# Kernel tuning notes

Measured on AMD Instinct MI355X. Metric: run time of the kernel, lower is better.

Reference implementation:

```python
import jax, jax.numpy as jnp
import numpy as np

B, T_ENC, T_DEC = 64, 256, 200
MEL, R = 80, 2
ENC_DIM = 256   # must equal attention_context_dim (context = weighted sum of encoder outputs)
ATT = 256       # attention_rnn_units == attention_context_dim
DEC = 256       # decoder_rnn_units
PRE1, PRE2 = 256, 128


def _gru(x, h, wih, whh, bih, bhh):
    # torch.nn.GRUCell math; weights are (3*H, in) torch layout
    gi = x @ wih.T + bih
    gh = h @ whh.T + bhh
    i_r, i_z, i_n = jnp.split(gi, 3, axis=-1)
    h_r, h_z, h_n = jnp.split(gh, 3, axis=-1)
    r = jax.nn.sigmoid(i_r + h_r)
    z = jax.nn.sigmoid(i_z + h_z)
    n = jnp.tanh(i_n + r * h_n)
    return (1.0 - z) * n + z * h


def setup_inputs() -> dict:
    key = jax.random.key(0)
    ks = iter(jax.random.split(key, 40))
    def nrm(shape, s=0.05):
        return jax.random.normal(next(ks), shape, dtype=jnp.float32) * s
    inp = {
        "encoder_outputs": nrm((B, T_ENC, ENC_DIM), 1.0),
        "inputs": nrm((B, T_DEC, MEL * R), 1.0),
        "memory_lengths": jax.random.randint(next(ks), (B,), T_ENC // 2, T_ENC + 1),
        # prenet
        "pre_w1": nrm((PRE1, MEL * R)), "pre_b1": jnp.zeros((PRE1,), jnp.float32),
        "pre_w2": nrm((PRE2, PRE1)),    "pre_b2": jnp.zeros((PRE2,), jnp.float32),
        # memory layer (no bias)
        "mem_w": nrm((ATT, ENC_DIM)),
        # attention GRUCell: input = prenet_out(128) + context(256)
        "att_wih": nrm((3 * ATT, PRE2 + ATT)), "att_whh": nrm((3 * ATT, ATT)),
        "att_bih": jnp.zeros((3 * ATT,), jnp.float32), "att_bhh": jnp.zeros((3 * ATT,), jnp.float32),
        # Bahdanau attention: query layer (no bias) and v vector
        "q_w": nrm((ATT, ATT)), "v_w": nrm((ATT,)),
        # project_to_decoder_in
        "proj_w": nrm((DEC, ATT + ATT)), "proj_b": jnp.zeros((DEC,), jnp.float32),
        # two decoder GRUCells
        "g1_wih": nrm((3 * DEC, DEC)), "g1_whh": nrm((3 * DEC, DEC)),
        "g1_bih": jnp.zeros((3 * DEC,), jnp.float32), "g1_bhh": jnp.zeros((3 * DEC,), jnp.float32),
        "g2_wih": nrm((3 * DEC, DEC)), "g2_whh": nrm((3 * DEC, DEC)),
        "g2_bih": jnp.zeros((3 * DEC,), jnp.float32), "g2_bhh": jnp.zeros((3 * DEC,), jnp.float32),
        # output projections
        "mel_w": nrm((MEL * R, DEC + ATT)), "mel_b": jnp.zeros((MEL * R,), jnp.float32),
        "stop_w": nrm((1, DEC + ATT)),      "stop_b": jnp.zeros((1,), jnp.float32),
    }
    return inp


def reference(encoder_outputs, inputs, memory_lengths,
              pre_w1, pre_b1, pre_w2, pre_b2, mem_w,
              att_wih, att_whh, att_bih, att_bhh, q_w, v_w,
              proj_w, proj_b,
              g1_wih, g1_whh, g1_bih, g1_bhh,
              g2_wih, g2_whh, g2_bih, g2_bhh,
              mel_w, mel_b, stop_w, stop_b):
    b = encoder_outputs.shape[0]
    processed_memory = encoder_outputs @ mem_w.T                    # (B,T_enc,ATT)
    pad_mask = jnp.arange(T_ENC)[None, :] >= memory_lengths[:, None]  # True = padding

    # teacher forcing: step t consumes previous target frame (zeros at t=0)
    x_seq = jnp.concatenate([jnp.zeros((b, 1, MEL * R), inputs.dtype), inputs[:, :-1]], axis=1)
    xs = jnp.swapaxes(x_seq, 0, 1)                                  # (T_dec,B,mel*r)

    def step(carry, x):
        h_att, ctx, h1, h2 = carry
        # prenet (dropout omitted: deterministic reference)
        pre = jax.nn.relu(jax.nn.relu(x @ pre_w1.T + pre_b1) @ pre_w2.T + pre_b2)
        # attention RNN
        h_att = _gru(jnp.concatenate([pre, ctx], -1), h_att, att_wih, att_whh, att_bih, att_bhh)
        # Bahdanau alignment
        score = jnp.einsum('btd,d->bt', jnp.tanh(processed_memory + (h_att @ q_w.T)[:, None, :]), v_w)
        score = jnp.where(pad_mask, -jnp.inf, score)
        align = jax.nn.softmax(score, axis=-1)                      # (B,T_enc)
        ctx = jnp.einsum('bt,btd->bd', align, encoder_outputs)      # (B,ATT)
        # decoder stack with residuals
        d = jnp.concatenate([h_att, ctx], -1) @ proj_w.T + proj_b
        h1 = _gru(d, h1, g1_wih, g1_whh, g1_bih, g1_bhh); d = h1 + d
        h2 = _gru(d, h2, g2_wih, g2_whh, g2_bih, g2_bhh); d = h2 + d
        p = jnp.concatenate([d, ctx], -1)
        mel = p @ mel_w.T + mel_b                                   # (B,mel*r)
        stop = jax.nn.sigmoid(p @ stop_w.T + stop_b)[:, 0]          # (B,)
        return (h_att, ctx, h1, h2), (mel, align, stop)

    zeros = lambda d: jnp.zeros((b, d), encoder_outputs.dtype)
    init = (zeros(ATT), zeros(ATT), zeros(DEC), zeros(DEC))
    _, (mels, aligns, stops) = jax.lax.scan(step, init, xs)

    mel_outputs = jnp.swapaxes(mels, 0, 1)                          # (B,T_dec,mel*r)
    attn_scores = jnp.swapaxes(aligns, 0, 1)                        # (B,T_dec,T_enc)
    stop_tokens = jnp.repeat(jnp.swapaxes(stops, 0, 1), R, axis=1)  # (B,T_dec*r)
    return mel_outputs, attn_scores, stop_tokens
```

## Files before the change

### kernel.cpp

```cpp
#include <hip/hip_runtime.h>
#include <math.h>
#include <stdint.h>

#define NB   64
#define TE   256
#define TD   200
#define MR   160

typedef _Float16 h2 __attribute__((ext_vector_type(2)));

__device__ __forceinline__ float dot2f(h2 a, h2 b, float c){
  return __builtin_amdgcn_fdot2(a, b, c, false);
}
__device__ __forceinline__ h2 u2h(unsigned int u){ return __builtin_bit_cast(h2, u); }
__device__ __forceinline__ unsigned int h2u(h2 h){ return __builtin_bit_cast(unsigned int, h); }

__device__ __forceinline__ float sigmf(float x){
  return __fdividef(1.f, 1.f + __expf(-x));
}
__device__ __forceinline__ float tanhf_(float x){
  float ax = fabsf(x);
  float e  = __expf(-2.f*ax);
  float r  = __fdividef(1.f - e, 1.f + e);
  return copysignf(r, x);
}

static constexpr size_t OFF_PM   = 0;
static constexpr size_t OFF_ENCH = 8388608;
static constexpr size_t OFF_GIP  = 16777216;
static constexpr size_t OFF_P    = 36438016;
static constexpr size_t OFF_W2   = 49545216;
static constexpr size_t OFF_W8   = 50184192;
static constexpr size_t WS_NEEDED = 52936704;

static constexpr size_t A_PW1  = 0;
static constexpr size_t A_PW2  = 20480;
static constexpr size_t A_WIHP = 36864;
static constexpr size_t A_MEMW = 86016;
static constexpr size_t A_MELW = 118784;

static constexpr size_t B_ATTC = 0;
static constexpr size_t B_ATTH = 24576;
static constexpr size_t B_G1I  = 49152;
static constexpr size_t B_G1H  = 73728;
static constexpr size_t B_G2I  = 98304;
static constexpr size_t B_G2H  = 122880;
static constexpr size_t B_PROJ = 147456;
static constexpr size_t B_QW   = 163840;

__global__ void k_conv(const float* __restrict__ src, char* __restrict__ ws,
                       unsigned off_h2, int O, int Kh, int k0, int ld){
  int i = blockIdx.x*256 + threadIdx.x;
  if (i >= O*Kh) return;
  int o = i % O, kp = i / O;
  _Float16* dst = (_Float16*)(ws + OFF_W2) + 2*((size_t)off_h2 + i);
  dst[0] = (_Float16)src[(size_t)o*ld + k0 + 2*kp    ];
  dst[1] = (_Float16)src[(size_t)o*ld + k0 + 2*kp + 1];
}

__global__ void k_conv8(const float* __restrict__ src, char* __restrict__ ws,
                        unsigned off16, int O, int Kq, int k0, int ld){
  int i = blockIdx.x*256 + threadIdx.x;
  if (i >= O*Kq) return;
  int o = i % O, kq = i / O;
  const float* s = src + (size_t)o*ld + k0 + kq*8;
  h2 p0, p1, p2, p3;
  p0.x=(_Float16)s[0]; p0.y=(_Float16)s[1];
  p1.x=(_Float16)s[2]; p1.y=(_Float16)s[3];
  p2.x=(_Float16)s[4]; p2.y=(_Float16)s[5];
  p3.x=(_Float16)s[6]; p3.y=(_Float16)s[7];
  uint4 r; r.x=h2u(p0); r.y=h2u(p1); r.z=h2u(p2); r.w=h2u(p3);
  ((uint4*)(ws + OFF_W8))[(size_t)off16 + i] = r;
}

__global__ void k_pm(const float* __restrict__ enc, char* __restrict__ ws){
  int bt = blockIdx.x;
  int j  = threadIdx.x;
  const h2* mw = (const h2*)(ws + OFF_W2) + A_MEMW;
  _Float16* pmN  = (_Float16*)(ws + OFF_PM);
  _Float16* encH = (_Float16*)(ws + OFF_ENCH);
  __shared__ _Float16 e[256];
  float ev = enc[(size_t)bt*256 + j];
  e[j] = (_Float16)ev;
  encH[(size_t)bt*256 + j] = (_Float16)ev;
  __syncthreads();
  const h2* e2 = (const h2*)e;
  float acc = 0.f;
  #pragma unroll 8
  for (int kp=0; kp<128; ++kp) acc = dot2f(mw[kp*256 + j], e2[kp], acc);
  pmN[(size_t)bt*256 + j] = (_Float16)acc;
}

__global__ void k_pre(const float* __restrict__ xin, const float* __restrict__ b1,
                      const float* __restrict__ b2, const float* __restrict__ bih,
                      char* __restrict__ ws){
  int bt = blockIdx.x;
  int b = bt / TD, t = bt % TD;
  int j = threadIdx.x;
  const h2* w1 = (const h2*)(ws + OFF_W2) + A_PW1;
  const h2* w2 = (const h2*)(ws + OFF_W2) + A_PW2;
  const h2* wp = (const h2*)(ws + OFF_W2) + A_WIHP;
  _Float16* gip = (_Float16*)(ws + OFF_GIP) + (size_t)bt*768;
  __shared__ _Float16 xh[160];
  __shared__ _Float16 a1[256];
  __shared__ _Float16 pr[128];
  if (j < 160)
    xh[j] = (t==0) ? (_Float16)0.f : (_Float16)xin[((size_t)b*TD + (t-1))*MR + j];
  __syncthreads();
  {
    const h2* x2 = (const h2*)xh;
    float acc = b1[j];
    #pragma unroll 8
    for (int kp=0; kp<80; ++kp) acc = dot2f(w1[kp*256 + j], x2[kp], acc);
    a1[j] = (_Float16)fmaxf(acc, 0.f);
  }
  __syncthreads();
  if (j < 128){
    const h2* x2 = (const h2*)a1;
    float acc = b2[j];
    #pragma unroll 8
    for (int kp=0; kp<128; ++kp) acc = dot2f(w2[kp*128 + j], x2[kp], acc);
    pr[j] = (_Float16)fmaxf(acc, 0.f);
  }
  __syncthreads();
  {
    const h2* p2 = (const h2*)pr;
    for (int o=j; o<768; o+=256){
      float acc = bih[o];
      #pragma unroll 8
      for (int kp=0; kp<64; ++kp) acc = dot2f(wp[kp*768 + o], p2[kp], acc);
      gip[o] = (_Float16)acc;
    }
  }
}

__global__ void k_zero(float* __restrict__ out){
  int* prog = (int*)(out + (size_t)NB*TD*MR + (size_t)NB*TD*TE);
  if (threadIdx.x < 256) prog[threadIdx.x] = 0;
}

__device__ __forceinline__ float d4dot(uint4 w, uint4 x, float a){
  a = dot2f(u2h(w.x), u2h(x.x), a);
  a = dot2f(u2h(w.y), u2h(x.y), a);
  a = dot2f(u2h(w.z), u2h(x.z), a);
  a = dot2f(u2h(w.w), u2h(x.w), a);
  return a;
}

__device__ __forceinline__ void gemv4(const uint4* __restrict__ wI, const uint4* __restrict__ wH,
                                      const uint4* xI, const uint4* xH,
                                      int j, int ks, float* scr, int tid){
  float a0=0.f,a1=0.f,a2=0.f,a3=0.f;
  #pragma unroll 2
  for (int kq=ks*8; kq<ks*8+8; ++kq){
    uint4 xi = xI[kq];
    uint4 xh = xH[kq];
    a0 = d4dot(wI[kq*768 +       j], xi, a0);
    a1 = d4dot(wI[kq*768 + 256 + j], xi, a1);
    a2 = d4dot(wI[kq*768 + 512 + j], xi, a2);
    a0 = d4dot(wH[kq*768 +       j], xh, a0);
    a1 = d4dot(wH[kq*768 + 256 + j], xh, a1);
    a3 = d4dot(wH[kq*768 + 512 + j], xh, a3);
  }
  float* r = scr + tid*4;
  r[0]=a0; r[1]=a1; r[2]=a2; r[3]=a3;
}

__global__ __launch_bounds__(1024) void k_dec(
    const int*   __restrict__ memlen,
    const float* __restrict__ att_bhh,
    const float* __restrict__ vw,
    const float* __restrict__ proj_b,
    const float* __restrict__ g1_bih, const float* __restrict__ g1_bhh,
    const float* __restrict__ g2_bih, const float* __restrict__ g2_bhh,
    float* __restrict__ out, char* __restrict__ ws)
{
  const int tid  = threadIdx.x;
  const int x    = blockIdx.x;
  const int y    = x >> 3;
  const int role = y & 3;
  const int b    = ((y >> 2) << 3) | (x & 7);
  const int ks   = tid >> 8;
  const int j    = tid & 255;

  const uint4* W8 = (const uint4*)(ws + OFF_W8);
  int* prog = (int*)(out + (size_t)NB*TD*MR + (size_t)NB*TD*TE);
  int* pCtx = prog + 64;
  int* pD   = prog + 128;
  int* pB1  = prog + 192;
  unsigned* gX = (unsigned*)((_Float16*)(ws + OFF_GIP) + (size_t)b*TD*768);

  __shared__ __align__(16) _Float16 hAh[256], ctxh[256], hh[256], dh[256];
  __shared__ float hAf[256], hf[256], df[256];
  __shared__ float qf[256], sc[256], al[256], vl[256];
  __shared__ float scr[4096];
  __shared__ float red2[4];
  __shared__ __align__(16) uint4 pmL[8192];

  if (role == 0){
    const uint4* wAC = W8 + B_ATTC;
    const uint4* wAH = W8 + B_ATTH;
    const uint4* wQ4 = W8 + B_QW;
    const uint4* pm4 = (const uint4*)(ws + OFF_PM) + (size_t)b*8192;
    const unsigned* encW = (const unsigned*)(ws + OFF_ENCH) + (size_t)b*TE*128;
    const _Float16* gipB = (const _Float16*)(ws + OFF_GIP) + (size_t)b*TD*768;
    _Float16* pstB = (_Float16*)(ws + OFF_P) + (size_t)b*TD*512;
    float* outA = out + (size_t)NB*TD*MR + (size_t)b*TD*TE;
    const int ml = memlen[b];
    const int tsl = tid>>7, dp = tid&127;

    for (int idx = tid; idx < 8192; idx += 1024){
      int tp = idx >> 5, g = idx & 31;
      pmL[(tp<<5) | (g ^ (tp & 7))] = pm4[idx];
    }
    if (tid < 256){ hAh[tid]=(_Float16)0.f; hAf[tid]=0.f; ctxh[tid]=(_Float16)0.f; vl[tid]=vw[tid]; }
    __syncthreads();
    const uint4* hA4  = (const uint4*)hAh;
    const uint4* ctx4 = (const uint4*)ctxh;

    #pragma unroll 1
    for (int t=0; t<TD; ++t){
      gemv4(wAC, wAH, ctx4, hA4, j, ks, scr, tid);
      __syncthreads();
      if (tid < 256){
        const _Float16* gp = gipB + (size_t)t*768;
        float s0 = scr[tid*4+0]+scr[(256+tid)*4+0]+scr[(512+tid)*4+0]+scr[(768+tid)*4+0];
        float s1 = scr[tid*4+1]+scr[(256+tid)*4+1]+scr[(512+tid)*4+1]+scr[(768+tid)*4+1];
        float s2 = scr[tid*4+2]+scr[(256+tid)*4+2]+scr[(512+tid)*4+2]+scr[(768+tid)*4+2];
        float s3 = scr[tid*4+3]+scr[(256+tid)*4+3]+scr[(512+tid)*4+3]+scr[(768+tid)*4+3];
        float r = sigmf(s0 + (float)gp[tid]     + att_bhh[tid]);
        float z = sigmf(s1 + (float)gp[256+tid] + att_bhh[256+tid]);
        float n = tanhf_(s2 + (float)gp[512+tid] + r*(s3 + att_bhh[512+tid]));
        float h = (1.f-z)*n + z*hAf[tid];
        hAf[tid]=h; hAh[tid]=(_Float16)h;
      }
      __syncthreads();
      { float a=0.f;
        #pragma unroll 2
        for (int kq=ks*8; kq<ks*8+8; ++kq)
          a = d4dot(wQ4[kq*256 + j], hA4[kq], a);
        scr[tid]=a; }
      __syncthreads();
      if (tid<256) qf[tid] = scr[tid]+scr[256+tid]+scr[512+tid]+scr[768+tid];
      __syncthreads();
      { float s=0.f;
        #pragma unroll
        for (int i=0;i<8;++i){
          int g = ks*8 + i;
          uint4 q4 = pmL[(j<<5) | (g ^ (j&7))];
          int d0 = ks*64 + i*8;
          h2 p0=u2h(q4.x), p1=u2h(q4.y), p2=u2h(q4.z), p3=u2h(q4.w);
          s += vl[d0+0]*tanhf_((float)p0.x + qf[d0+0]);
          s += vl[d0+1]*tanhf_((float)p0.y + qf[d0+1]);
          s += vl[d0+2]*tanhf_((float)p1.x + qf[d0+2]);
          s += vl[d0+3]*tanhf_((float)p1.y + qf[d0+3]);
          s += vl[d0+4]*tanhf_((float)p2.x + qf[d0+4]);
          s += vl[d0+5]*tanhf_((float)p2.y + qf[d0+5]);
          s += vl[d0+6]*tanhf_((float)p3.x + qf[d0+6]);
          s += vl[d0+7]*tanhf_((float)p3.y + qf[d0+7]);
        }
        scr[tid]=s; }
      __syncthreads();
      if (tid<256){
        float s = scr[tid]+scr[256+tid]+scr[512+tid]+scr[768+tid];
        sc[tid] = (tid < ml) ? s : -INFINITY;
      }
      __syncthreads();
      {
        float v = (tid<256) ? sc[tid] : -INFINITY;
        if (tid<256){
          #pragma unroll
          for (int o=32;o>0;o>>=1) v = fmaxf(v, __shfl_down(v,o,64));
          if ((tid&63)==0) red2[tid>>6]=v;
        }
        __syncthreads();
        float m = fmaxf(fmaxf(red2[0],red2[1]), fmaxf(red2[2],red2[3]));
        __syncthreads();
        float e = 0.f;
        if (tid<256){
          e = __expf(sc[tid]-m);
          float sv = e;
          #pragma unroll
          for (int o=32;o>0;o>>=1) sv += __shfl_down(sv,o,64);
          if ((tid&63)==0) red2[tid>>6]=sv;
        }
        __syncthreads();
        if (tid<256){
          float sum = red2[0]+red2[1]+red2[2]+red2[3];
          float a = e*__fdividef(1.f,sum);
          al[tid]=a;
          outA[(size_t)t*TE + tid]=a;
        }
      }
      __syncthreads();
      { float c0=0.f, c1=0.f;
        #pragma unroll 8
        for (int tp=tsl*32; tp<tsl*32+32; ++tp){
          float a = al[tp];
          h2 e = u2h(encW[(size_t)tp*128 + dp]);
          c0 += a*(float)e.x; c1 += a*(float)e.y;
        }
        scr[tid*2]=c0; scr[tid*2+1]=c1; }
      __syncthreads();
      if (tid<128){
        float c0=0.f, c1=0.f;
        #pragma unroll
        for (int k=0;k<8;++k){ c0 += scr[(k*128+tid)*2]; c1 += scr[(k*128+tid)*2+1]; }
        h2 c; c.x=(_Float16)c0; c.y=(_Float16)c1;
        unsigned w = h2u(c);
        ((unsigned*)ctxh)[tid] = w;
        ((unsigned*)pstB)[(size_t)t*256 + 128 + tid] = w;
        __hip_atomic_store(gX + (size_t)t*384 + tid, ((const unsigned*)hAh)[tid],
                           __ATOMIC_RELAXED, __HIP_MEMORY_SCOPE_AGENT);
        __hip_atomic_store(gX + (size_t)t*384 + 128 + tid, w,
                           __ATOMIC_RELAXED, __HIP_MEMORY_SCOPE_AGENT);
      }
      __syncthreads();
      if (tid==0)
        __hip_atomic_store(pCtx+b, t+1, __ATOMIC_RELEASE, __HIP_MEMORY_SCOPE_AGENT);
    }
  } else if (role == 1){
    const uint4* wPRJ = W8 + B_PROJ;
    const uint4* hA4  = (const uint4*)hAh;
    const uint4* ctx4 = (const uint4*)ctxh;

    #pragma unroll 1
    for (int t=0; t<TD; ++t){
      if (tid==0){
        while (__hip_atomic_load(pCtx+b, __ATOMIC_RELAXED, __HIP_MEMORY_SCOPE_AGENT) < t+1)
          __builtin_amdgcn_s_sleep(1);
      }
      __syncthreads();
      if (tid<256){
        unsigned w = __hip_atomic_load(gX + (size_t)t*384 + tid,
                                       __ATOMIC_RELAXED, __HIP_MEMORY_SCOPE_AGENT);
        if (tid<128) ((unsigned*)hAh)[tid] = w;
        else         ((unsigned*)ctxh)[tid-128] = w;
      }
      __syncthreads();
      { float a=0.f;
        #pragma unroll 2
        for (int kq=ks*16; kq<ks*16+16; ++kq){
          uint4 xa = (kq < 32) ? hA4[kq] : ctx4[kq-32];
          a = d4dot(wPRJ[kq*256 + j], xa, a);
        }
        scr[tid]=a; }
      __syncthreads();
      if (tid<128){
        const int o0 = 2*tid, o1 = o0+1;
        float d0 = scr[o0]+scr[256+o0]+scr[512+o0]+scr[768+o0] + proj_b[o0];
        float d1 = scr[o1]+scr[256+o1]+scr[512+o1]+scr[768+o1] + proj_b[o1];
        h2 p; p.x=(_Float16)d0; p.y=(_Float16)d1;
        __hip_atomic_store(gX + (size_t)t*384 + 256 + tid, h2u(p),
                           __ATOMIC_RELAXED, __HIP_MEMORY_SCOPE_AGENT);
      }
      __syncthreads();
      if (tid==0)
        __hip_atomic_store(pD+b, t+1, __ATOMIC_RELEASE, __HIP_MEMORY_SCOPE_AGENT);
    }
  } else {
    const bool isB1 = (role == 2);
    const uint4* wI = W8 + (isB1 ? B_G1I : B_G2I);
    const uint4* wH = W8 + (isB1 ? B_G1H : B_G2H);
    const float* bih = isB1 ? g1_bih : g2_bih;
    const float* bhh = isB1 ? g1_bhh : g2_bhh;
    int* pin = isB1 ? pD : pB1;
    unsigned* oX = (unsigned*)out + (size_t)b*TD*128;
    const unsigned* inP = isB1 ? (gX + 256) : oX;
    const int instr = isB1 ? 384 : 128;
    _Float16* pstB = (_Float16*)(ws + OFF_P) + (size_t)b*TD*512;

    if (tid<256){ hh[tid]=(_Float16)0.f; hf[tid]=0.f; }
    __syncthreads();
    const uint4* h4  = (const uint4*)hh;
    const uint4* dd4 = (const uint4*)dh;

    #pragma unroll 1
    for (int t=0; t<TD; ++t){
      if (tid==0){
        while (__hip_atomic_load(pin+b, __ATOMIC_RELAXED, __HIP_MEMORY_SCOPE_AGENT) < t+1)
          __builtin_amdgcn_s_sleep(1);
      }
      __syncthreads();
      if (tid<128){
        unsigned w = __hip_atomic_load(inP + (size_t)t*instr + tid,
                                       __ATOMIC_RELAXED, __HIP_MEMORY_SCOPE_AGENT);
        ((unsigned*)dh)[tid] = w;
        h2 p = u2h(w);
        df[2*tid]   = (float)p.x;
        df[2*tid+1] = (float)p.y;
      }
      __syncthreads();
      gemv4(wI, wH, dd4, h4, j, ks, scr, tid);
      __syncthreads();
      if (tid<256){
        float s0 = scr[tid*4+0]+scr[(256+tid)*4+0]+scr[(512+tid)*4+0]+scr[(768+tid)*4+0];
        float s1 = scr[tid*4+1]+scr[(256+tid)*4+1]+scr[(512+tid)*4+1]+scr[(768+tid)*4+1];
        float s2 = scr[tid*4+2]+scr[(256+tid)*4+2]+scr[(512+tid)*4+2]+scr[(768+tid)*4+2];
        float s3 = scr[tid*4+3]+scr[(256+tid)*4+3]+scr[(512+tid)*4+3]+scr[(768+tid)*4+3];
        float r = sigmf(s0 + bih[tid]     + bhh[tid]);
        float z = sigmf(s1 + bih[256+tid] + bhh[256+tid]);
        float n = tanhf_(s2 + bih[512+tid] + r*(s3 + bhh[512+tid]));
        float h = (1.f-z)*n + z*hf[tid];
        float dn = h + df[tid];
        hf[tid]=h; hh[tid]=(_Float16)h;
        dh[tid]=(_Float16)dn;
        if (!isB1) pstB[(size_t)t*512 + tid] = (_Float16)dn;
      }
      __syncthreads();
      if (isB1){
        if (tid<128)
          __hip_atomic_store(oX + (size_t)t*128 + tid, ((const unsigned*)dh)[tid],
                             __ATOMIC_RELAXED, __HIP_MEMORY_SCOPE_AGENT);
        __syncthreads();
        if (tid==0)
          __hip_atomic_store(pB1+b, t+1, __ATOMIC_RELEASE, __HIP_MEMORY_SCOPE_AGENT);
      }
    }
  }
}

__global__ void k_post(const float* __restrict__ mel_b, const float* __restrict__ stop_w,
                       const float* __restrict__ stop_b, float* __restrict__ out,
                       char* __restrict__ ws){
  int bt = blockIdx.x;
  int b = bt / TD, t = bt % TD;
  int j = threadIdx.x;
  const h2* wm = (const h2*)(ws + OFF_W2) + A_MELW;
  const _Float16* p = (const _Float16*)(ws + OFF_P) + (size_t)bt*512;
  __shared__ _Float16 pl[512];
  ((uint32_t*)pl)[j] = ((const uint32_t*)p)[j];
  __syncthreads();
  const h2* p2 = (const h2*)pl;
  if (j < 160){
    float acc = mel_b[j];
    #pragma unroll 8
    for (int kp=0; kp<256; ++kp) acc = dot2f(wm[kp*160 + j], p2[kp], acc);
    out[(size_t)bt*MR + j] = acc;
  } else if (j == 160){
    float acc = stop_b[0];
    for (int k=0; k<512; ++k) acc += stop_w[k]*(float)pl[k];
    float s = __fdividef(1.f, 1.f + __expf(-acc));
    float* os = out + (size_t)NB*TD*MR + (size_t)NB*TD*TE + (size_t)b*2*TD;
    os[2*t]   = s;
    os[2*t+1] = s;
  }
}

extern "C" void kernel_launch(void* const* d_in, const int* in_sizes, int n_in,
                              void* d_out, int out_size, void* d_ws, size_t ws_size,
                              hipStream_t stream)
{
  const float* enc     = (const float*)d_in[0];
  const float* xin     = (const float*)d_in[1];
  const int*   mlen    = (const int*)  d_in[2];
  const float* pre_w1  = (const float*)d_in[3];
  const float* pre_b1  = (const float*)d_in[4];
  const float* pre_w2  = (const float*)d_in[5];
  const float* pre_b2  = (const float*)d_in[6];
  const float* mem_w   = (const float*)d_in[7];
  const float* att_wih = (const float*)d_in[8];
  const float* att_whh = (const float*)d_in[9];
  const float* att_bih = (const float*)d_in[10];
  const float* att_bhh = (const float*)d_in[11];
  const float* q_w     = (const float*)d_in[12];
  const float* v_w     = (const float*)d_in[13];
  const float* proj_w  = (const float*)d_in[14];
  const float* proj_b  = (const float*)d_in[15];
  const float* g1_wih  = (const float*)d_in[16];
  const float* g1_whh  = (const float*)d_in[17];
  const float* g1_bih  = (const float*)d_in[18];
  const float* g1_bhh  = (const float*)d_in[19];
  const float* g2_wih  = (const float*)d_in[20];
  const float* g2_whh  = (const float*)d_in[21];
  const float* g2_bih  = (const float*)d_in[22];
  const float* g2_bhh  = (const float*)d_in[23];
  const float* mel_w   = (const float*)d_in[24];
  const float* mel_b   = (const float*)d_in[25];
  const float* stop_w  = (const float*)d_in[26];
  const float* stop_b  = (const float*)d_in[27];
  (void)in_sizes; (void)n_in; (void)out_size;

  if (ws_size < WS_NEEDED) return;

  float* out = (float*)d_out;
  char*  ws  = (char*)d_ws;

  auto conv = [&](const float* src, size_t off_h2, int O, int Kh, int k0, int ld){
    int n = O*Kh;
    k_conv<<<(n+255)/256, 256, 0, stream>>>(src, ws, (unsigned)off_h2, O, Kh, k0, ld);
  };
  auto conv8 = [&](const float* src, size_t off16, int O, int Kq, int k0, int ld){
    int n = O*Kq;
    k_conv8<<<(n+255)/256, 256, 0, stream>>>(src, ws, (unsigned)off16, O, Kq, k0, ld);
  };

  conv(pre_w1,  A_PW1,  256, 80,  0, 160);
  conv(pre_w2,  A_PW2,  128, 128, 0, 256);
  conv(att_wih, A_WIHP, 768, 64,  0, 384);
  conv(mem_w,   A_MEMW, 256, 128, 0, 256);
  conv(mel_w,   A_MELW, 160, 256, 0, 512);
  conv8(att_wih, B_ATTC, 768, 32, 128, 384);
  conv8(att_whh, B_ATTH, 768, 32, 0,   256);
  conv8(g1_wih,  B_G1I,  768, 32, 0,   256);
  conv8(g1_whh,  B_G1H,  768, 32, 0,   256);
  conv8(g2_wih,  B_G2I,  768, 32, 0,   256);
  conv8(g2_whh,  B_G2H,  768, 32, 0,   256);
  conv8(proj_w,  B_PROJ, 256, 64, 0,   512);
  conv8(q_w,     B_QW,   256, 32, 0,   256);

  k_pm  <<<NB*TE, 256, 0, stream>>>(enc, ws);
  k_pre <<<NB*TD, 256, 0, stream>>>(xin, pre_b1, pre_b2, att_bih, ws);
  k_zero<<<1, 256, 0, stream>>>(out);
  k_dec <<<4*NB, 1024, 0, stream>>>(mlen, att_bhh, v_w, proj_b,
                                    g1_bih, g1_bhh, g2_bih, g2_bhh, out, ws);
  k_post<<<NB*TD, 256, 0, stream>>>(mel_b, stop_w, stop_b, out, ws);
}
```

Baseline: 5.105 ms.

## Offload most of the attention-GRU context GEMV to the projection block

Splits the attention GRU's input-side GEMV over the context vector. The role-0 block now computes only the hidden-state part plus the first 64 context elements. The role-1 block computes the remaining context contributions right after receiving ctx, publishes the partial gate sums through a global slot, and signals them with a new progress flag. The aim is to shorten the serial critical path in the attention block by overlapping that work with the other role. The cost is an extra cross-block spin-wait and global round trip every step, and the scratch slot reuses a region of the output buffer.

After: 5.103 ms. No clear change (-0.1%).

```diff
diff --git a/kernel.cpp b/kernel.cpp
--- a/kernel.cpp
+++ b/kernel.cpp
@@ -14,6 +14,8 @@
 }
 __device__ __forceinline__ h2 u2h(unsigned int u){ return __builtin_bit_cast(h2, u); }
 __device__ __forceinline__ unsigned int h2u(h2 h){ return __builtin_bit_cast(unsigned int, h); }
+__device__ __forceinline__ unsigned f2u(float f){ return __builtin_bit_cast(unsigned, f); }
+__device__ __forceinline__ float u2f(unsigned u){ return __builtin_bit_cast(float, u); }
 
 __device__ __forceinline__ float sigmf(float x){
   return __fdividef(1.f, 1.f + __expf(-x));
@@ -166,6 +168,30 @@
   r[0]=a0; r[1]=a1; r[2]=a2; r[3]=a3;
 }
 
+__device__ __forceinline__ void gemvA(const uint4* __restrict__ wAC, const uint4* __restrict__ wAH,
+                                      const uint4* xc, const uint4* xh,
+                                      int j, int ks, float* scr, int tid){
+  float a0=0.f,a1=0.f,a2=0.f,a3=0.f;
+  #pragma unroll 2
+  for (int i=0;i<8;++i){
+    int kq = ks*8+i;
+    uint4 xv = xh[kq];
+    a0 = d4dot(wAH[kq*768 +       j], xv, a0);
+    a1 = d4dot(wAH[kq*768 + 256 + j], xv, a1);
+    a3 = d4dot(wAH[kq*768 + 512 + j], xv, a3);
+  }
+  #pragma unroll
+  for (int i=0;i<2;++i){
+    int kq = ks*2+i;
+    uint4 xv = xc[kq];
+    a0 = d4dot(wAC[kq*768 +       j], xv, a0);
+    a1 = d4dot(wAC[kq*768 + 256 + j], xv, a1);
+    a2 = d4dot(wAC[kq*768 + 512 + j], xv, a2);
+  }
+  float* r = scr + tid*4;
+  r[0]=a0; r[1]=a1; r[2]=a2; r[3]=a3;
+}
+
 __global__ __launch_bounds__(1024) void k_dec(
     const int*   __restrict__ memlen,
     const float* __restrict__ att_bhh,
@@ -185,10 +211,12 @@
 
   const uint4* W8 = (const uint4*)(ws + OFF_W8);
   int* prog = (int*)(out + (size_t)NB*TD*MR + (size_t)NB*TD*TE);
+  int* pGP  = prog;
   int* pCtx = prog + 64;
   int* pD   = prog + 128;
   int* pB1  = prog + 192;
   unsigned* gX = (unsigned*)((_Float16*)(ws + OFF_GIP) + (size_t)b*TD*768);
+  unsigned* uSlot = (unsigned*)(out + (size_t)NB*TD*128) + (size_t)b*768;
 
   __shared__ __align__(16) _Float16 hAh[256], ctxh[256], hh[256], dh[256];
   __shared__ float hAf[256], hf[256], df[256];
@@ -220,7 +248,11 @@
 
     #pragma unroll 1
     for (int t=0; t<TD; ++t){
-      gemv4(wAC, wAH, ctx4, hA4, j, ks, scr, tid);
+      gemvA(wAC, wAH, ctx4, hA4, j, ks, scr, tid);
+      if (t > 0 && tid==0){
+        while (__hip_atomic_load(pGP+b, __ATOMIC_RELAXED, __HIP_MEMORY_SCOPE_AGENT) < t)
+          __builtin_amdgcn_s_sleep(1);
+      }
       __syncthreads();
       if (tid < 256){
         const _Float16* gp = gipB + (size_t)t*768;
@@ -228,6 +260,11 @@
         float s1 = scr[tid*4+1]+scr[(256+tid)*4+1]+scr[(512+tid)*4+1]+scr[(768+tid)*4+1];
         float s2 = scr[tid*4+2]+scr[(256+tid)*4+2]+scr[(512+tid)*4+2]+scr[(768+tid)*4+2];
         float s3 = scr[tid*4+3]+scr[(256+tid)*4+3]+scr[(512+tid)*4+3]+scr[(768+tid)*4+3];
+        if (t > 0){
+          s0 += u2f(__hip_atomic_load(uSlot +       tid, __ATOMIC_RELAXED, __HIP_MEMORY_SCOPE_AGENT));
+          s1 += u2f(__hip_atomic_load(uSlot + 256 + tid, __ATOMIC_RELAXED, __HIP_MEMORY_SCOPE_AGENT));
+          s2 += u2f(__hip_atomic_load(uSlot + 512 + tid, __ATOMIC_RELAXED, __HIP_MEMORY_SCOPE_AGENT));
+        }
         float r = sigmf(s0 + (float)gp[tid]     + att_bhh[tid]);
         float z = sigmf(s1 + (float)gp[256+tid] + att_bhh[256+tid]);
         float n = tanhf_(s2 + (float)gp[512+tid] + r*(s3 + att_bhh[512+tid]));
@@ -320,6 +357,7 @@
         __hip_atomic_store(pCtx+b, t+1, __ATOMIC_RELEASE, __HIP_MEMORY_SCOPE_AGENT);
     }
   } else if (role == 1){
+    const uint4* wAC  = W8 + B_ATTC;
     const uint4* wPRJ = W8 + B_PROJ;
     const uint4* hA4  = (const uint4*)hAh;
     const uint4* ctx4 = (const uint4*)ctxh;
@@ -338,6 +376,28 @@
         else         ((unsigned*)ctxh)[tid-128] = w;
       }
       __syncthreads();
+      { float a0=0.f, a1=0.f, a2=0.f;
+        #pragma unroll 2
+        for (int i=0;i<6;++i){
+          int kq = 8 + ks*6 + i;
+          uint4 xv = ctx4[kq];
+          a0 = d4dot(wAC[kq*768 +       j], xv, a0);
+          a1 = d4dot(wAC[kq*768 + 256 + j], xv, a1);
+          a2 = d4dot(wAC[kq*768 + 512 + j], xv, a2);
+        }
+        float* r = scr + tid*3; r[0]=a0; r[1]=a1; r[2]=a2; }
+      __syncthreads();
+      if (tid<256){
+        float p0 = scr[tid*3+0]+scr[(256+tid)*3+0]+scr[(512+tid)*3+0]+scr[(768+tid)*3+0];
+        float p1 = scr[tid*3+1]+scr[(256+tid)*3+1]+scr[(512+tid)*3+1]+scr[(768+tid)*3+1];
+        float p2 = scr[tid*3+2]+scr[(256+tid)*3+2]+scr[(512+tid)*3+2]+scr[(768+tid)*3+2];
+        __hip_atomic_store(uSlot +       tid, f2u(p0), __ATOMIC_RELAXED, __HIP_MEMORY_SCOPE_AGENT);
+        __hip_atomic_store(uSlot + 256 + tid, f2u(p1), __ATOMIC_RELAXED, __HIP_MEMORY_SCOPE_AGENT);
+        __hip_atomic_store(uSlot + 512 + tid, f2u(p2), __ATOMIC_RELAXED, __HIP_MEMORY_SCOPE_AGENT);
+      }
+      __syncthreads();
+      if (tid==0)
+        __hip_atomic_store(pGP+b, t+1, __ATOMIC_RELEASE, __HIP_MEMORY_SCOPE_AGENT);
       { float a=0.f;
         #pragma unroll 2
         for (int kq=ks*16; kq<ks*16+16; ++kq){
```
